# Optimization experiments

Measured on AMD Instinct MI355X. Metric: run time of the kernel, lower is better.

The kernel has to match this reference:

```python
import jax, jax.numpy as jnp
import numpy as np

H, W = 448, 448
C = 32
HEADS = 2
HEAD_DIM = C // HEADS
B, N = 4, 20000
SHIFTS = jnp.array([[0, 0], [-1, 0], [1, 0], [0, 1], [-1, 1], [1, 1], [0, -1], [-1, -1], [1, -1]], dtype=jnp.int32)  # [9,2]


def _layer_norm(x, w, b):
    mu = x.mean(-1, keepdims=True)
    var = ((x - mu) ** 2).mean(-1, keepdims=True)
    return (x - mu) / jnp.sqrt(var + 1e-5) * w + b


def _direction(q_feat, q_coor, kv_feat, kv_coor, qkv_w, qkv_b, in_w, in_b, out_w, out_b, pos_w, pos_b):
    # q_feat: [N,C] (already layer-normed), q_coor/kv_coor: [N,2] int (y,x)
    n = q_feat.shape[0]
    q_map = q_feat @ qkv_w[0].T + qkv_b[0]   # 1x1 conv == linear
    k_map = kv_feat @ qkv_w[1].T + qkv_b[1]
    v_map = kv_feat @ qkv_w[2].T + qkv_b[2]
    # dense coordinate -> voxel-index lookup table for the kv modality
    lut = jnp.full(H * W, -1, dtype=jnp.int32)
    lut = lut.at[kv_coor[:, 0] * W + kv_coor[:, 1]].set(jnp.arange(kv_coor.shape[0], dtype=jnp.int32))
    shifted = q_coor[:, None, :] + SHIFTS[None]                      # [N,9,2]
    inb = ((shifted >= 0) & (shifted < jnp.array([H, W]))).all(-1)   # [N,9]
    flat = jnp.clip(shifted[..., 0], 0, H - 1) * W + jnp.clip(shifted[..., 1], 0, W - 1)
    idx = jnp.where(inb, lut[flat], -1)                              # [N,9], -1 = no match
    mask = idx >= 0
    gi = jnp.maximum(idx, 0)
    pos = SHIFTS.astype(q_feat.dtype) @ pos_w.T + pos_b              # [9,C]
    v_g = jnp.where(mask[..., None], v_map[gi] + pos[None], 0.0)     # [N,9,C]
    k_g = jnp.where(mask[..., None], k_map[gi], 0.0)                 # [N,9,C]
    # MultiheadAttention (eval): 1 query token over 9 neighbor tokens, per voxel
    wq, wk, wv = in_w[:C], in_w[C:2 * C], in_w[2 * C:]
    bq, bk, bv = in_b[:C], in_b[C:2 * C], in_b[2 * C:]
    q = (q_map @ wq.T + bq).reshape(n, HEADS, HEAD_DIM)
    k = (k_g @ wk.T + bk).reshape(n, 9, HEADS, HEAD_DIM)
    v = (v_g @ wv.T + bv).reshape(n, 9, HEADS, HEAD_DIM)
    scores = jnp.einsum('nhd,nkhd->nhk', q, k) / jnp.sqrt(jnp.asarray(HEAD_DIM, q.dtype))
    attn = jax.nn.softmax(scores, axis=-1)
    o = jnp.einsum('nhk,nkhd->nhd', attn, v).reshape(n, C)
    out = o @ out_w.T + out_b                                        # [N,C]
    # scatter into BEV pseudoimage
    canvas = jnp.zeros((H * W, C), out.dtype).at[q_coor[:, 0] * W + q_coor[:, 1]].set(out)
    return canvas.T.reshape(C, H, W)


def setup_inputs() -> dict:
    key = jax.random.key(0)
    ks = jax.random.split(key, 20)
    rng = np.random.default_rng(0)
    def coords(rng):
        flat = np.stack([rng.choice(H * W, size=N, replace=False) for _ in range(B)])
        return jnp.asarray(np.stack([flat // W, flat % W], axis=-1), dtype=jnp.int32)  # [B,N,2]
    s = 0.05
    return {
        'li_feats': jax.random.normal(ks[0], (B, N, C), jnp.float32),
        'ra_feats': jax.random.normal(ks[1], (B, N, C), jnp.float32),
        'li_coors': coords(rng),
        'ra_coors': coords(rng),
        'li_norm_w': jnp.ones((C,), jnp.float32),
        'li_norm_b': jnp.zeros((C,), jnp.float32),
        'ra_norm_w': jnp.ones((C,), jnp.float32),
        'ra_norm_b': jnp.zeros((C,), jnp.float32),
        'qkv1_w': jax.random.normal(ks[2], (3, C, C), jnp.float32) * s,
        'qkv1_b': jax.random.normal(ks[3], (3, C), jnp.float32) * s,
        'qkv2_w': jax.random.normal(ks[4], (3, C, C), jnp.float32) * s,
        'qkv2_b': jax.random.normal(ks[5], (3, C), jnp.float32) * s,
        'pos_w': jax.random.normal(ks[6], (C, 2), jnp.float32) * s,
        'pos_b': jax.random.normal(ks[7], (C,), jnp.float32) * s,
        'attn1_in_w': jax.random.normal(ks[8], (3 * C, C), jnp.float32) * s,
        'attn1_in_b': jax.random.normal(ks[9], (3 * C,), jnp.float32) * s,
        'attn1_out_w': jax.random.normal(ks[10], (C, C), jnp.float32) * s,
        'attn1_out_b': jax.random.normal(ks[11], (C,), jnp.float32) * s,
        'attn2_in_w': jax.random.normal(ks[12], (3 * C, C), jnp.float32) * s,
        'attn2_in_b': jax.random.normal(ks[13], (3 * C,), jnp.float32) * s,
        'attn2_out_w': jax.random.normal(ks[14], (C, C), jnp.float32) * s,
        'attn2_out_b': jax.random.normal(ks[15], (C,), jnp.float32) * s,
    }


def reference(li_feats, ra_feats, li_coors, ra_coors, li_norm_w, li_norm_b, ra_norm_w, ra_norm_b,
              qkv1_w, qkv1_b, qkv2_w, qkv2_b, pos_w, pos_b,
              attn1_in_w, attn1_in_b, attn1_out_w, attn1_out_b,
              attn2_in_w, attn2_in_b, attn2_out_w, attn2_out_b):
    li_n = _layer_norm(li_feats, li_norm_w, li_norm_b)  # [B,N,C]
    ra_n = _layer_norm(ra_feats, ra_norm_w, ra_norm_b)
    d1 = jax.vmap(lambda qf, qc, kf, kc: _direction(qf, qc, kf, kc, qkv1_w, qkv1_b,
                                                    attn1_in_w, attn1_in_b, attn1_out_w, attn1_out_b, pos_w, pos_b))
    d2 = jax.vmap(lambda qf, qc, kf, kc: _direction(qf, qc, kf, kc, qkv2_w, qkv2_b,
                                                    attn2_in_w, attn2_in_b, attn2_out_w, attn2_out_b, pos_w, pos_b))
    li_img = d1(li_n, li_coors, ra_n, ra_coors)  # [B,C,H,W]
    ra_img = d2(ra_n, ra_coors, li_n, li_coors)  # [B,C,H,W]
    return li_img, ra_img
```

## Files before the change

### kernel.cpp

```cpp
#include <hip/hip_runtime.h>
#include <hip/hip_bf16.h>

#define HH 448
#define WW 448
#define HWP (HH*WW)
#define CC 32
#define NN 20000
#define BB 4
#define NPB 79

__constant__ int c_SY[9] = {0,-1,1,0,-1,1,0,-1,1};
__constant__ int c_SX[9] = {0,0,0,1,1,1,-1,-1,-1};

#define WB_STRIDE 4608

static __device__ __forceinline__ float bf(const __hip_bfloat16 v) {
    return __bfloat162float(v);
}
static __device__ __forceinline__ float ldf(const void* p, int i, int isf32) {
    if (isf32) return ((const float*)p)[i];
    return __bfloat162float(((const __hip_bfloat16*)p)[i]);
}
static __device__ __forceinline__ float blo(unsigned int u) { return __uint_as_float((u & 0xFFFFu) << 16); }
static __device__ __forceinline__ float bhi(unsigned int u) { return __uint_as_float(u & 0xFFFF0000u); }

static __device__ __forceinline__ void unpack8(uint4 r, float* f) {
    f[0]=blo(r.x); f[1]=bhi(r.x); f[2]=blo(r.y); f[3]=bhi(r.y);
    f[4]=blo(r.z); f[5]=bhi(r.z); f[6]=blo(r.w); f[7]=bhi(r.w);
}
static __device__ __forceinline__ float dot8(uint4 r, const float* q) {
    float a = 0.f;
    a = fmaf(blo(r.x), q[0], a); a = fmaf(bhi(r.x), q[1], a);
    a = fmaf(blo(r.y), q[2], a); a = fmaf(bhi(r.y), q[3], a);
    a = fmaf(blo(r.z), q[4], a); a = fmaf(bhi(r.z), q[5], a);
    a = fmaf(blo(r.w), q[6], a); a = fmaf(bhi(r.w), q[7], a);
    return a;
}
static __device__ __forceinline__ void acc8(uint4 r, float w, float4 pA, float4 pB, float* o) {
    o[0]=fmaf(w, blo(r.x)+pA.x, o[0]); o[1]=fmaf(w, bhi(r.x)+pA.y, o[1]);
    o[2]=fmaf(w, blo(r.y)+pA.z, o[2]); o[3]=fmaf(w, bhi(r.y)+pA.w, o[3]);
    o[4]=fmaf(w, blo(r.z)+pB.x, o[4]); o[5]=fmaf(w, bhi(r.z)+pB.y, o[5]);
    o[6]=fmaf(w, blo(r.w)+pB.z, o[6]); o[7]=fmaf(w, bhi(r.w)+pB.w, o[7]);
}
static __device__ __forceinline__ void store32bf(__hip_bfloat16* p, const float* a) {
    __hip_bfloat16 h[32];
    #pragma unroll
    for (int c = 0; c < 32; ++c) h[c] = __float2bfloat16(a[c]);
    uint4* rp = (uint4*)p; const uint4* hp = (const uint4*)h;
    rp[0] = hp[0]; rp[1] = hp[1]; rp[2] = hp[2]; rp[3] = hp[3];
}

__launch_bounds__(256)
__global__ void prep_build(const void* __restrict__ qkv1_w, const void* __restrict__ qkv1_b,
                           const void* __restrict__ qkv2_w, const void* __restrict__ qkv2_b,
                           const void* __restrict__ pos_w,  const void* __restrict__ pos_b,
                           const void* __restrict__ in1_w,  const void* __restrict__ in1_b,
                           const void* __restrict__ out1_w, const void* __restrict__ out1_b,
                           const void* __restrict__ in2_w,  const void* __restrict__ in2_b,
                           const void* __restrict__ out2_w, const void* __restrict__ out2_b,
                           const void* __restrict__ li_feats,
                           const int* __restrict__ li_coors, const int* __restrict__ ra_coors,
                           int* __restrict__ lut,
                           int* __restrict__ flag, float* __restrict__ wsW) {
    const int tid = threadIdx.x;
    if (blockIdx.x >= 2) {
        const int t = (blockIdx.x - 2) * 256 + tid;
        if (t >= 2 * BB * NN) return;
        const int tensor = t / (BB * NN);
        const int r = t % (BB * NN);
        const int b = r / NN, n = r % NN;
        const int* cc = tensor ? ra_coors : li_coors;
        const int y = cc[(size_t)(b * NN + n) * 2 + 0];
        const int x = cc[(size_t)(b * NN + n) * 2 + 1];
        lut[(size_t)(tensor * BB + b) * HWP + y * WW + x] = n;
        return;
    }
    __shared__ int cnt[256];
    {
        const unsigned short u = ((const unsigned short*)li_feats)[tid * 2];
        const int e = (u >> 7) & 0xFF;
        cnt[tid] = (u == 0 || (e >= 97 && e <= 157)) ? 1 : 0;
    }
    __syncthreads();
    for (int s = 128; s > 0; s >>= 1) {
        if (tid < s) cnt[tid] += cnt[tid + s];
        __syncthreads();
    }
    const int F = (cnt[0] >= 192) ? 0 : 1;
    if (blockIdx.x == 0 && tid == 0) *flag = F;

    const int d = blockIdx.x;
    const void* qw  = d ? qkv2_w : qkv1_w;
    const void* qb  = d ? qkv2_b : qkv1_b;
    const void* iw  = d ? in2_w  : in1_w;
    const void* ib  = d ? in2_b  : in1_b;
    const void* ow  = d ? out2_w : out1_w;
    const void* obp = d ? out2_b : out1_b;
    float* o = wsW + d * WB_STRIDE;

    __shared__ float s_qw[3072];
    __shared__ float s_iw[96 * 33];
    __shared__ float s_ow[32 * 33];
    __shared__ float s_qb[96], s_ib[96], s_obp[32], s_pw[64], s_pb[32];

    if (F) {
        const float* fqw = (const float*)qw;  const float* fiw = (const float*)iw;
        const float* fow = (const float*)ow;  const float* fqb = (const float*)qb;
        const float* fib = (const float*)ib;  const float* fob = (const float*)obp;
        const float* fpw = (const float*)pos_w; const float* fpb = (const float*)pos_b;
        for (int i = tid; i < 3072; i += 256) s_qw[i] = fqw[i];
        for (int i = tid; i < 3072; i += 256) s_iw[(i >> 5) * 33 + (i & 31)] = fiw[i];
        for (int i = tid; i < 1024; i += 256) s_ow[(i >> 5) * 33 + (i & 31)] = fow[i];
        if (tid < 96) { s_qb[tid] = fqb[tid]; s_ib[tid] = fib[tid]; }
        if (tid < 64) s_pw[tid] = fpw[tid];
        if (tid < 32) { s_obp[tid] = fob[tid]; s_pb[tid] = fpb[tid]; }
    } else {
        const __hip_bfloat16* hqw = (const __hip_bfloat16*)qw;  const __hip_bfloat16* hiw = (const __hip_bfloat16*)iw;
        const __hip_bfloat16* how = (const __hip_bfloat16*)ow;  const __hip_bfloat16* hqb = (const __hip_bfloat16*)qb;
        const __hip_bfloat16* hib = (const __hip_bfloat16*)ib;  const __hip_bfloat16* hob = (const __hip_bfloat16*)obp;
        const __hip_bfloat16* hpw = (const __hip_bfloat16*)pos_w; const __hip_bfloat16* hpb = (const __hip_bfloat16*)pos_b;
        for (int i = tid; i < 3072; i += 256) s_qw[i] = bf(hqw[i]);
        for (int i = tid; i < 3072; i += 256) s_iw[(i >> 5) * 33 + (i & 31)] = bf(hiw[i]);
        for (int i = tid; i < 1024; i += 256) s_ow[(i >> 5) * 33 + (i & 31)] = bf(how[i]);
        if (tid < 96) { s_qb[tid] = bf(hqb[tid]); s_ib[tid] = bf(hib[tid]); }
        if (tid < 64) s_pw[tid] = bf(hpw[tid]);
        if (tid < 32) { s_obp[tid] = bf(hob[tid]); s_pb[tid] = bf(hpb[tid]); }
    }
    __syncthreads();

    for (int k = 0; k < 4; ++k) {
        const int idx = tid + k * 256;
        const int t = idx >> 5, i = idx & 31;
        float aq = 0.f, ak = 0.f, av = 0.f;
        #pragma unroll
        for (int u = 0; u < 32; ++u) {
            const float q0 = s_qw[u * 32 + t];
            const float q1 = s_qw[1024 + u * 32 + t];
            const float q2 = s_qw[2048 + u * 32 + t];
            aq = fmaf(s_iw[i * 33 + u],        q0, aq);
            ak = fmaf(s_iw[(32 + i) * 33 + u], q1, ak);
            av = fmaf(s_iw[(64 + i) * 33 + u], q2, av);
        }
        o[idx]        = aq;
        o[1024 + idx] = ak;
        o[2048 + idx] = av;
        o[3072 + idx] = s_ow[i * 33 + t];
    }
    if (tid < 32) {
        const int i = tid;
        float aq = 0.f, ak = 0.f, av = 0.f;
        #pragma unroll
        for (int u = 0; u < 32; ++u) {
            aq = fmaf(s_qb[u],      s_iw[i * 33 + u],        aq);
            ak = fmaf(s_qb[32 + u], s_iw[(32 + i) * 33 + u], ak);
            av = fmaf(s_qb[64 + u], s_iw[(64 + i) * 33 + u], av);
        }
        o[4096 + i] = aq + s_ib[i];
        o[4128 + i] = ak + s_ib[32 + i];
        o[4160 + i] = av + s_ib[64 + i];
        o[4192 + i] = s_obp[i];
        o[4224 + i] = s_ib[32 + i];
        o[4256 + i] = s_ib[64 + i];
    }
    for (int idx = tid; idx < 288; idx += 256) {
        const int s = idx >> 5, i = idx & 31;
        const float sy = (float)c_SY[s], sx = (float)c_SX[s];
        float acc = 0.f;
        #pragma unroll
        for (int j = 0; j < 32; ++j) {
            const float pj = sy * s_pw[j * 2 + 0] + sx * s_pw[j * 2 + 1] + s_pb[j];
            acc = fmaf(pj, s_iw[(64 + i) * 33 + j], acc);
        }
        o[4288 + idx] = acc;
    }
}

__launch_bounds__(256)
__global__ void project_kernel(const void* __restrict__ li_feats, const void* __restrict__ ra_feats,
                               const void* __restrict__ li_nw, const void* __restrict__ li_nb,
                               const void* __restrict__ ra_nw, const void* __restrict__ ra_nb,
                               const int* __restrict__ flag, const float* __restrict__ wsW,
                               __hip_bfloat16* __restrict__ qOut, __hip_bfloat16* __restrict__ kOut,
                               __hip_bfloat16* __restrict__ vOut) {
    const int F = *flag;
    const int combo  = blockIdx.x / NPB;
    const int n      = (blockIdx.x % NPB) * 256 + threadIdx.x;
    if (n >= NN) return;
    const int tensor = combo >> 2;
    const int b      = combo & 3;
    const float* Wq  = wsW + tensor * WB_STRIDE;
    const float* Wkv = wsW + (1 - tensor) * WB_STRIDE;

    const void* feats = tensor ? ra_feats : li_feats;
    const void* nwp   = tensor ? ra_nw : li_nw;
    const void* nbp   = tensor ? ra_nb : li_nb;

    float x[32];
    if (F) {
        const float4* fr = (const float4*)((const float*)feats + (size_t)(b * NN + n) * CC);
        #pragma unroll
        for (int i = 0; i < 8; ++i) {
            const float4 t = fr[i];
            x[4*i] = t.x; x[4*i+1] = t.y; x[4*i+2] = t.z; x[4*i+3] = t.w;
        }
    } else {
        const uint4* hr = (const uint4*)((const __hip_bfloat16*)feats + (size_t)(b * NN + n) * CC);
        unpack8(hr[0], x); unpack8(hr[1], x + 8);
        unpack8(hr[2], x + 16); unpack8(hr[3], x + 24);
    }
    float s = 0.f;
    #pragma unroll
    for (int c = 0; c < 32; ++c) s += x[c];
    const float mu = s * (1.f / 32.f);
    float s2 = 0.f;
    #pragma unroll
    for (int c = 0; c < 32; ++c) { const float dx = x[c] - mu; s2 += dx * dx; }
    const float rs = rsqrtf(s2 * (1.f / 32.f) + 1e-5f);
    #pragma unroll
    for (int c = 0; c < 32; ++c)
        x[c] = (x[c] - mu) * rs * ldf(nwp, c, F) + ldf(nbp, c, F);

    const size_t off = ((size_t)(tensor * BB + b) * NN + n) * CC;
    #pragma unroll
    for (int pass = 0; pass < 3; ++pass) {
        const float* W = (pass == 0) ? Wq : Wkv + pass * 1024;
        const float* Bv = (pass == 0) ? (Wq + 4096) : (Wkv + 4096 + pass * 32);
        float a[32];
        const float4* b4 = (const float4*)Bv;
        #pragma unroll
        for (int i4 = 0; i4 < 8; ++i4) {
            const float4 t = b4[i4];
            a[4*i4] = t.x; a[4*i4+1] = t.y; a[4*i4+2] = t.z; a[4*i4+3] = t.w;
        }
        #pragma unroll
        for (int j = 0; j < 32; ++j) {
            const float xj = x[j];
            const float4* wr = (const float4*)&W[j * 32];
            #pragma unroll
            for (int i4 = 0; i4 < 8; ++i4) {
                const float4 w = wr[i4];
                a[4*i4+0] = fmaf(xj, w.x, a[4*i4+0]);
                a[4*i4+1] = fmaf(xj, w.y, a[4*i4+1]);
                a[4*i4+2] = fmaf(xj, w.z, a[4*i4+2]);
                a[4*i4+3] = fmaf(xj, w.w, a[4*i4+3]);
            }
        }
        store32bf((pass == 0 ? qOut : pass == 1 ? kOut : vOut) + off, a);
    }
}

__launch_bounds__(256)
__global__ void attn_kernel(const int* __restrict__ li_coors, const int* __restrict__ ra_coors,
                            const float* __restrict__ wsW, const int* __restrict__ lut,
                            const __hip_bfloat16* __restrict__ qArr, const __hip_bfloat16* __restrict__ kArr,
                            const __hip_bfloat16* __restrict__ vArr, __hip_bfloat16* __restrict__ resArr) {
    const int combo = blockIdx.x / NPB;
    const int n     = (blockIdx.x % NPB) * 256 + threadIdx.x;
    if (n >= NN) return;
    const int d = combo >> 2;
    const int b = combo & 3;
    const int qt = d, kt = 1 - d;
    const float* Wd = wsW + d * WB_STRIDE;

    const int* qc = qt ? ra_coors : li_coors;
    const int* lutk = lut + (size_t)(kt * BB + b) * HWP;
    const __hip_bfloat16* kk = kArr + (size_t)(kt * BB + b) * NN * CC;
    const __hip_bfloat16* vv = vArr + (size_t)(kt * BB + b) * NN * CC;
    const __hip_bfloat16* qq = qArr + (size_t)(qt * BB + b) * NN * CC;
    __hip_bfloat16* res = resArr + (size_t)(d * BB + b) * NN * CC;

    float q[32];
    {
        const uint4* qr = (const uint4*)(qq + (size_t)n * CC);
        unpack8(qr[0], q); unpack8(qr[1], q + 8);
        unpack8(qr[2], q + 16); unpack8(qr[3], q + 24);
    }
    const int y = qc[(size_t)(b * NN + n) * 2 + 0];
    const int x = qc[(size_t)(b * NN + n) * 2 + 1];
    int idx[9];
    #pragma unroll
    for (int s = 0; s < 9; ++s) {
        const int ny = y + c_SY[s], nx = x + c_SX[s];
        idx[s] = (ny >= 0 && ny < HH && nx >= 0 && nx < WW) ? lutk[ny * WW + nx] : -1;
    }
    float di0 = 0.f, di1 = 0.f;
    #pragma unroll
    for (int c = 0; c < 16; ++c) di0 = fmaf(q[c], Wd[4224 + c], di0);
    #pragma unroll
    for (int c = 16; c < 32; ++c) di1 = fmaf(q[c], Wd[4224 + c], di1);

    float s0[9], s1[9];
    #pragma unroll
    for (int s = 0; s < 9; ++s) {
        float d0, d1;
        if (idx[s] >= 0) {
            const uint4* kr = (const uint4*)(kk + (size_t)idx[s] * CC);
            const uint4 r0 = kr[0], r1 = kr[1], r2 = kr[2], r3 = kr[3];
            d0 = dot8(r0, q) + dot8(r1, q + 8);
            d1 = dot8(r2, q + 16) + dot8(r3, q + 24);
        } else { d0 = di0; d1 = di1; }
        s0[s] = d0 * 0.25f;
        s1[s] = d1 * 0.25f;
    }
    float m0 = s0[0], m1 = s1[0];
    #pragma unroll
    for (int s = 1; s < 9; ++s) { m0 = fmaxf(m0, s0[s]); m1 = fmaxf(m1, s1[s]); }
    float e0[9], e1[9], den0 = 0.f, den1 = 0.f;
    #pragma unroll
    for (int s = 0; s < 9; ++s) {
        e0[s] = __expf(s0[s] - m0); den0 += e0[s];
        e1[s] = __expf(s1[s] - m1); den1 += e1[s];
    }
    const float i0 = 1.f / den0, i1 = 1.f / den1;

    float o[32];
    #pragma unroll
    for (int c = 0; c < 32; ++c) o[c] = 0.f;
    float wi0 = 0.f, wi1 = 0.f;
    const float4* pv4 = (const float4*)&Wd[4288];
    #pragma unroll
    for (int s = 0; s < 9; ++s) {
        const float w0 = e0[s] * i0, w1 = e1[s] * i1;
        if (idx[s] >= 0) {
            const uint4* vr = (const uint4*)(vv + (size_t)idx[s] * CC);
            const uint4 r0 = vr[0], r1 = vr[1], r2 = vr[2], r3 = vr[3];
            acc8(r0, w0, pv4[s * 8 + 0], pv4[s * 8 + 1], o);
            acc8(r1, w0, pv4[s * 8 + 2], pv4[s * 8 + 3], o + 8);
            acc8(r2, w1, pv4[s * 8 + 4], pv4[s * 8 + 5], o + 16);
            acc8(r3, w1, pv4[s * 8 + 6], pv4[s * 8 + 7], o + 24);
        } else { wi0 += w0; wi1 += w1; }
    }
    #pragma unroll
    for (int c = 0; c < 16; ++c) o[c] = fmaf(wi0, Wd[4256 + c], o[c]);
    #pragma unroll
    for (int c = 16; c < 32; ++c) o[c] = fmaf(wi1, Wd[4256 + c], o[c]);

    float out[32];
    const float4* ob4 = (const float4*)&Wd[4192];
    #pragma unroll
    for (int i4 = 0; i4 < 8; ++i4) {
        const float4 t = ob4[i4];
        out[i4*4+0] = t.x; out[i4*4+1] = t.y;
        out[i4*4+2] = t.z; out[i4*4+3] = t.w;
    }
    #pragma unroll
    for (int j = 0; j < 32; ++j) {
        const float oj = o[j];
        const float4* wr = (const float4*)&Wd[3072 + j * 32];
        #pragma unroll
        for (int i4 = 0; i4 < 8; ++i4) {
            const float4 w = wr[i4];
            out[i4*4+0] = fmaf(oj, w.x, out[i4*4+0]);
            out[i4*4+1] = fmaf(oj, w.y, out[i4*4+1]);
            out[i4*4+2] = fmaf(oj, w.z, out[i4*4+2]);
            out[i4*4+3] = fmaf(oj, w.w, out[i4*4+3]);
        }
    }
    store32bf(res + (size_t)n * CC, out);
}

__launch_bounds__(256)
__global__ void canvas_kernel(const int* __restrict__ lut, const __hip_bfloat16* __restrict__ resArr,
                              const int* __restrict__ flag, void* __restrict__ out) {
    const int F = *flag;
    const int tile = blockIdx.x % (HWP / 64);
    const int rem  = blockIdx.x / (HWP / 64);
    const int b = rem & 3;
    const int d = rem >> 2;
    const int* lutq = lut + (size_t)(d * BB + b) * HWP + (size_t)tile * 64;
    __shared__ int ls[64];
    __shared__ float st[64 * 33];
    const int t = threadIdx.x;
    if (t < 16) ((int4*)ls)[t] = ((const int4*)lutq)[t];
    __syncthreads();

    const __hip_bfloat16* res = resArr + (size_t)(d * BB + b) * NN * CC;
    {
        const int r = t >> 2, q = t & 3;
        const int idx = ls[r];
        uint4 raw = make_uint4(0u, 0u, 0u, 0u);
        if (idx >= 0) raw = *(const uint4*)(res + (size_t)idx * CC + q * 8);
        float* dst = &st[r * 33 + q * 8];
        dst[0] = blo(raw.x); dst[1] = bhi(raw.x);
        dst[2] = blo(raw.y); dst[3] = bhi(raw.y);
        dst[4] = blo(raw.z); dst[5] = bhi(raw.z);
        dst[6] = blo(raw.w); dst[7] = bhi(raw.w);
    }
    __syncthreads();

    const int c = t >> 3, g = t & 7;
    float v[8];
    #pragma unroll
    for (int j = 0; j < 8; ++j) v[j] = st[(8 * g + j) * 33 + c];
    const size_t obase = ((size_t)(d * BB + b) * CC + c) * HWP + (size_t)tile * 64 + 8 * g;
    if (F) {
        float* ob = (float*)out + obase;
        ((float4*)ob)[0] = make_float4(v[0], v[1], v[2], v[3]);
        ((float4*)ob)[1] = make_float4(v[4], v[5], v[6], v[7]);
    } else {
        __hip_bfloat16* ob = (__hip_bfloat16*)out + obase;
        __hip_bfloat16 h[8];
        #pragma unroll
        for (int j = 0; j < 8; ++j) h[j] = __float2bfloat16(v[j]);
        *(uint4*)ob = *(const uint4*)h;
    }
}

extern "C" void kernel_launch(void* const* d_in, const int* in_sizes, int n_in,
                              void* d_out, int out_size, void* d_ws, size_t ws_size,
                              hipStream_t stream) {
    (void)in_sizes; (void)n_in; (void)out_size; (void)ws_size;
    const void* li_feats = d_in[0];
    const void* ra_feats = d_in[1];
    const int* li_coors = (const int*)d_in[2];
    const int* ra_coors = (const int*)d_in[3];
    const void* li_nw = d_in[4];
    const void* li_nb = d_in[5];
    const void* ra_nw = d_in[6];
    const void* ra_nb = d_in[7];

    char* ws = (char*)d_ws;
    int*   flag = (int*)ws;
    float* wsW  = (float*)(ws + 512);
    int*   lut  = (int*)(ws + 40960);
    __hip_bfloat16* qArr = (__hip_bfloat16*)(ws + 6463488);
    __hip_bfloat16* kArr = (__hip_bfloat16*)(ws + 16703488);
    __hip_bfloat16* vArr = (__hip_bfloat16*)(ws + 26943488);
    __hip_bfloat16* rArr = (__hip_bfloat16*)(ws + 37183488);

    hipMemsetAsync(lut, 0xFF, (size_t)2 * BB * HWP * sizeof(int), stream);
    const int buildBlocks = (2 * BB * NN + 255) / 256;
    prep_build<<<2 + buildBlocks, 256, 0, stream>>>(d_in[8], d_in[9], d_in[10], d_in[11], d_in[12], d_in[13],
                                                    d_in[14], d_in[15], d_in[16], d_in[17],
                                                    d_in[18], d_in[19], d_in[20], d_in[21],
                                                    li_feats, li_coors, ra_coors, lut, flag, wsW);
    project_kernel<<<8 * NPB, 256, 0, stream>>>(li_feats, ra_feats, li_nw, li_nb, ra_nw, ra_nb,
                                                flag, wsW, qArr, kArr, vArr);
    attn_kernel<<<8 * NPB, 256, 0, stream>>>(li_coors, ra_coors, wsW, lut, qArr, kArr, vArr, rArr);
    canvas_kernel<<<2 * BB * (HWP / 64), 256, 0, stream>>>(lut, rArr, flag, d_out);
}
```

Baseline: 334.9 us.

## Fuse Q projection into attention, interleave K/V, enlarge canvas tiles

The Q projection (layer norm plus matmul) now runs inside the attention kernel instead of going through a global bf16 buffer. K and V are stored interleaved per voxel as 64 contiguous values, so each neighbour gather reads one contiguous 128-byte row. This removes the Q write and read round trip and improves gather locality. The canvas kernel now covers 256 pixels per block in four sub-tiles, which cuts the block count and amortises the LUT load, at the cost of extra syncs per block.

Result: slower. 427.1 us (+27.5%).

```diff
diff --git a/kernel.cpp b/kernel.cpp
--- a/kernel.cpp
+++ b/kernel.cpp
@@ -48,6 +48,54 @@
     for (int c = 0; c < 32; ++c) h[c] = __float2bfloat16(a[c]);
     uint4* rp = (uint4*)p; const uint4* hp = (const uint4*)h;
     rp[0] = hp[0]; rp[1] = hp[1]; rp[2] = hp[2]; rp[3] = hp[3];
+}
+static __device__ __forceinline__ void mat32(const float* __restrict__ W, const float* __restrict__ Bv,
+                                             const float* x, float* a) {
+    const float4* b4 = (const float4*)Bv;
+    #pragma unroll
+    for (int i4 = 0; i4 < 8; ++i4) {
+        const float4 t = b4[i4];
+        a[4*i4] = t.x; a[4*i4+1] = t.y; a[4*i4+2] = t.z; a[4*i4+3] = t.w;
+    }
+    #pragma unroll
+    for (int j = 0; j < 32; ++j) {
+        const float xj = x[j];
+        const float4* wr = (const float4*)&W[j * 32];
+        #pragma unroll
+        for (int i4 = 0; i4 < 8; ++i4) {
+            const float4 w = wr[i4];
+            a[4*i4+0] = fmaf(xj, w.x, a[4*i4+0]);
+            a[4*i4+1] = fmaf(xj, w.y, a[4*i4+1]);
+            a[4*i4+2] = fmaf(xj, w.z, a[4*i4+2]);
+            a[4*i4+3] = fmaf(xj, w.w, a[4*i4+3]);
+        }
+    }
+}
+static __device__ __forceinline__ void load_ln(const void* feats, size_t row, int F,
+                                               const void* nwp, const void* nbp, float* x) {
+    if (F) {
+        const float4* fr = (const float4*)((const float*)feats + row * CC);
+        #pragma unroll
+        for (int i = 0; i < 8; ++i) {
+            const float4 t = fr[i];
+            x[4*i] = t.x; x[4*i+1] = t.y; x[4*i+2] = t.z; x[4*i+3] = t.w;
+        }
+    } else {
+        const uint4* hr = (const uint4*)((const __hip_bfloat16*)feats + row * CC);
+        unpack8(hr[0], x); unpack8(hr[1], x + 8);
+        unpack8(hr[2], x + 16); unpack8(hr[3], x + 24);
+    }
+    float s = 0.f;
+    #pragma unroll
+    for (int c = 0; c < 32; ++c) s += x[c];
+    const float mu = s * (1.f / 32.f);
+    float s2 = 0.f;
+    #pragma unroll
+    for (int c = 0; c < 32; ++c) { const float dx = x[c] - mu; s2 += dx * dx; }
+    const float rs = rsqrtf(s2 * (1.f / 32.f) + 1e-5f);
+    #pragma unroll
+    for (int c = 0; c < 32; ++c)
+        x[c] = (x[c] - mu) * rs * ldf(nwp, c, F) + ldf(nbp, c, F);
 }
 
 __launch_bounds__(256)
@@ -180,80 +228,38 @@
                                const void* __restrict__ li_nw, const void* __restrict__ li_nb,
                                const void* __restrict__ ra_nw, const void* __restrict__ ra_nb,
                                const int* __restrict__ flag, const float* __restrict__ wsW,
-                               __hip_bfloat16* __restrict__ qOut, __hip_bfloat16* __restrict__ kOut,
-                               __hip_bfloat16* __restrict__ vOut) {
+                               __hip_bfloat16* __restrict__ kvOut) {
     const int F = *flag;
     const int combo  = blockIdx.x / NPB;
     const int n      = (blockIdx.x % NPB) * 256 + threadIdx.x;
     if (n >= NN) return;
     const int tensor = combo >> 2;
     const int b      = combo & 3;
-    const float* Wq  = wsW + tensor * WB_STRIDE;
     const float* Wkv = wsW + (1 - tensor) * WB_STRIDE;
 
     const void* feats = tensor ? ra_feats : li_feats;
-    const void* nwp   = tensor ? ra_nw : li_nw;
-    const void* nbp   = tensor ? ra_nb : li_nb;
-
     float x[32];
-    if (F) {
-        const float4* fr = (const float4*)((const float*)feats + (size_t)(b * NN + n) * CC);
-        #pragma unroll
-        for (int i = 0; i < 8; ++i) {
-            const float4 t = fr[i];
-            x[4*i] = t.x; x[4*i+1] = t.y; x[4*i+2] = t.z; x[4*i+3] = t.w;
-        }
-    } else {
-        const uint4* hr = (const uint4*)((const __hip_bfloat16*)feats + (size_t)(b * NN + n) * CC);
-        unpack8(hr[0], x); unpack8(hr[1], x + 8);
-        unpack8(hr[2], x + 16); unpack8(hr[3], x + 24);
-    }
-    float s = 0.f;
-    #pragma unroll
-    for (int c = 0; c < 32; ++c) s += x[c];
-    const float mu = s * (1.f / 32.f);
-    float s2 = 0.f;
-    #pragma unroll
-    for (int c = 0; c < 32; ++c) { const float dx = x[c] - mu; s2 += dx * dx; }
-    const float rs = rsqrtf(s2 * (1.f / 32.f) + 1e-5f);
-    #pragma unroll
-    for (int c = 0; c < 32; ++c)
-        x[c] = (x[c] - mu) * rs * ldf(nwp, c, F) + ldf(nbp, c, F);
-
-    const size_t off = ((size_t)(tensor * BB + b) * NN + n) * CC;
-    #pragma unroll
-    for (int pass = 0; pass < 3; ++pass) {
-        const float* W = (pass == 0) ? Wq : Wkv + pass * 1024;
-        const float* Bv = (pass == 0) ? (Wq + 4096) : (Wkv + 4096 + pass * 32);
-        float a[32];
-        const float4* b4 = (const float4*)Bv;
-        #pragma unroll
-        for (int i4 = 0; i4 < 8; ++i4) {
-            const float4 t = b4[i4];
-            a[4*i4] = t.x; a[4*i4+1] = t.y; a[4*i4+2] = t.z; a[4*i4+3] = t.w;
-        }
-        #pragma unroll
-        for (int j = 0; j < 32; ++j) {
-            const float xj = x[j];
-            const float4* wr = (const float4*)&W[j * 32];
-            #pragma unroll
-            for (int i4 = 0; i4 < 8; ++i4) {
-                const float4 w = wr[i4];
-                a[4*i4+0] = fmaf(xj, w.x, a[4*i4+0]);
-                a[4*i4+1] = fmaf(xj, w.y, a[4*i4+1]);
-                a[4*i4+2] = fmaf(xj, w.z, a[4*i4+2]);
-                a[4*i4+3] = fmaf(xj, w.w, a[4*i4+3]);
-            }
-        }
-        store32bf((pass == 0 ? qOut : pass == 1 ? kOut : vOut) + off, a);
-    }
+    load_ln(feats, (size_t)(b * NN + n), F,
+            tensor ? ra_nw : li_nw, tensor ? ra_nb : li_nb, x);
+
+    const size_t off = ((size_t)(tensor * BB + b) * NN + n) * 64;
+    float a[32];
+    mat32(Wkv + 1024, Wkv + 4128, x, a);
+    store32bf(kvOut + off, a);
+    mat32(Wkv + 2048, Wkv + 4160, x, a);
+    store32bf(kvOut + off + 32, a);
 }
 
 __launch_bounds__(256)
-__global__ void attn_kernel(const int* __restrict__ li_coors, const int* __restrict__ ra_coors,
+__global__ void attn_kernel(const void* __restrict__ li_feats, const void* __restrict__ ra_feats,
+                            const void* __restrict__ li_nw, const void* __restrict__ li_nb,
+                            const void* __restrict__ ra_nw, const void* __restrict__ ra_nb,
+                            const int* __restrict__ li_coors, const int* __restrict__ ra_coors,
+                            const int* __restrict__ flag,
                             const float* __restrict__ wsW, const int* __restrict__ lut,
-                            const __hip_bfloat16* __restrict__ qArr, const __hip_bfloat16* __restrict__ kArr,
-                            const __hip_bfloat16* __restrict__ vArr, __hip_bfloat16* __restrict__ resArr) {
+                            const __hip_bfloat16* __restrict__ kvArr,
+                            __hip_bfloat16* __restrict__ resArr) {
+    const int F = *flag;
     const int combo = blockIdx.x / NPB;
     const int n     = (blockIdx.x % NPB) * 256 + threadIdx.x;
     if (n >= NN) return;
@@ -264,16 +270,15 @@
 
     const int* qc = qt ? ra_coors : li_coors;
     const int* lutk = lut + (size_t)(kt * BB + b) * HWP;
-    const __hip_bfloat16* kk = kArr + (size_t)(kt * BB + b) * NN * CC;
-    const __hip_bfloat16* vv = vArr + (size_t)(kt * BB + b) * NN * CC;
-    const __hip_bfloat16* qq = qArr + (size_t)(qt * BB + b) * NN * CC;
+    const __hip_bfloat16* kvb = kvArr + (size_t)(kt * BB + b) * NN * 64;
     __hip_bfloat16* res = resArr + (size_t)(d * BB + b) * NN * CC;
 
     float q[32];
     {
-        const uint4* qr = (const uint4*)(qq + (size_t)n * CC);
-        unpack8(qr[0], q); unpack8(qr[1], q + 8);
-        unpack8(qr[2], q + 16); unpack8(qr[3], q + 24);
+        float x[32];
+        load_ln(qt ? ra_feats : li_feats, (size_t)(b * NN + n), F,
+                qt ? ra_nw : li_nw, qt ? ra_nb : li_nb, x);
+        mat32(Wd, Wd + 4096, x, q);
     }
     const int y = qc[(size_t)(b * NN + n) * 2 + 0];
     const int x = qc[(size_t)(b * NN + n) * 2 + 1];
@@ -294,7 +299,7 @@
     for (int s = 0; s < 9; ++s) {
         float d0, d1;
         if (idx[s] >= 0) {
-            const uint4* kr = (const uint4*)(kk + (size_t)idx[s] * CC);
+            const uint4* kr = (const uint4*)(kvb + (size_t)idx[s] * 64);
             const uint4 r0 = kr[0], r1 = kr[1], r2 = kr[2], r3 = kr[3];
             d0 = dot8(r0, q) + dot8(r1, q + 8);
             d1 = dot8(r2, q + 16) + dot8(r3, q + 24);
@@ -322,7 +327,7 @@
     for (int s = 0; s < 9; ++s) {
         const float w0 = e0[s] * i0, w1 = e1[s] * i1;
         if (idx[s] >= 0) {
-            const uint4* vr = (const uint4*)(vv + (size_t)idx[s] * CC);
+            const uint4* vr = (const uint4*)(kvb + (size_t)idx[s] * 64 + 32);
             const uint4 r0 = vr[0], r1 = vr[1], r2 = vr[2], r3 = vr[3];
             acc8(r0, w0, pv4[s * 8 + 0], pv4[s * 8 + 1], o);
             acc8(r1, w0, pv4[s * 8 + 2], pv4[s * 8 + 3], o + 8);
@@ -336,26 +341,7 @@
     for (int c = 16; c < 32; ++c) o[c] = fmaf(wi1, Wd[4256 + c], o[c]);
 
     float out[32];
-    const float4* ob4 = (const float4*)&Wd[4192];
-    #pragma unroll
-    for (int i4 = 0; i4 < 8; ++i4) {
-        const float4 t = ob4[i4];
-        out[i4*4+0] = t.x; out[i4*4+1] = t.y;
-        out[i4*4+2] = t.z; out[i4*4+3] = t.w;
-    }
-    #pragma unroll
-    for (int j = 0; j < 32; ++j) {
-        const float oj = o[j];
-        const float4* wr = (const float4*)&Wd[3072 + j * 32];
-        #pragma unroll
-        for (int i4 = 0; i4 < 8; ++i4) {
-            const float4 w = wr[i4];
-            out[i4*4+0] = fmaf(oj, w.x, out[i4*4+0]);
-            out[i4*4+1] = fmaf(oj, w.y, out[i4*4+1]);
-            out[i4*4+2] = fmaf(oj, w.z, out[i4*4+2]);
-            out[i4*4+3] = fmaf(oj, w.w, out[i4*4+3]);
-        }
-    }
+    mat32(Wd + 3072, Wd + 4192, o, out);
     store32bf(res + (size_t)n * CC, out);
 }
 
@@ -363,46 +349,49 @@
 __global__ void canvas_kernel(const int* __restrict__ lut, const __hip_bfloat16* __restrict__ resArr,
                               const int* __restrict__ flag, void* __restrict__ out) {
     const int F = *flag;
-    const int tile = blockIdx.x % (HWP / 64);
-    const int rem  = blockIdx.x / (HWP / 64);
+    const int tile = blockIdx.x % (HWP / 256);
+    const int rem  = blockIdx.x / (HWP / 256);
     const int b = rem & 3;
     const int d = rem >> 2;
-    const int* lutq = lut + (size_t)(d * BB + b) * HWP + (size_t)tile * 64;
-    __shared__ int ls[64];
+    const int* lutq = lut + (size_t)(d * BB + b) * HWP + (size_t)tile * 256;
+    __shared__ int ls[256];
     __shared__ float st[64 * 33];
     const int t = threadIdx.x;
-    if (t < 16) ((int4*)ls)[t] = ((const int4*)lutq)[t];
-    __syncthreads();
+    if (t < 64) ((int4*)ls)[t] = ((const int4*)lutq)[t];
 
     const __hip_bfloat16* res = resArr + (size_t)(d * BB + b) * NN * CC;
-    {
-        const int r = t >> 2, q = t & 3;
-        const int idx = ls[r];
-        uint4 raw = make_uint4(0u, 0u, 0u, 0u);
-        if (idx >= 0) raw = *(const uint4*)(res + (size_t)idx * CC + q * 8);
-        float* dst = &st[r * 33 + q * 8];
-        dst[0] = blo(raw.x); dst[1] = bhi(raw.x);
-        dst[2] = blo(raw.y); dst[3] = bhi(raw.y);
-        dst[4] = blo(raw.z); dst[5] = bhi(raw.z);
-        dst[6] = blo(raw.w); dst[7] = bhi(raw.w);
-    }
-    __syncthreads();
-
+    const size_t cbase = (size_t)(d * BB + b) * CC * HWP + (size_t)tile * 256;
+    const int r = t >> 2, qc4 = t & 3;
     const int c = t >> 3, g = t & 7;
-    float v[8];
-    #pragma unroll
-    for (int j = 0; j < 8; ++j) v[j] = st[(8 * g + j) * 33 + c];
-    const size_t obase = ((size_t)(d * BB + b) * CC + c) * HWP + (size_t)tile * 64 + 8 * g;
-    if (F) {
-        float* ob = (float*)out + obase;
-        ((float4*)ob)[0] = make_float4(v[0], v[1], v[2], v[3]);
-        ((float4*)ob)[1] = make_float4(v[4], v[5], v[6], v[7]);
-    } else {
-        __hip_bfloat16* ob = (__hip_bfloat16*)out + obase;
-        __hip_bfloat16 h[8];
-        #pragma unroll
-        for (int j = 0; j < 8; ++j) h[j] = __float2bfloat16(v[j]);
-        *(uint4*)ob = *(const uint4*)h;
+
+    for (int sub = 0; sub < 4; ++sub) {
+        __syncthreads();
+        {
+            const int idx = ls[sub * 64 + r];
+            uint4 raw = make_uint4(0u, 0u, 0u, 0u);
+            if (idx >= 0) raw = *(const uint4*)(res + (size_t)idx * CC + qc4 * 8);
+            float* dst = &st[r * 33 + qc4 * 8];
+            dst[0] = blo(raw.x); dst[1] = bhi(raw.x);
+            dst[2] = blo(raw.y); dst[3] = bhi(raw.y);
+            dst[4] = blo(raw.z); dst[5] = bhi(raw.z);
+            dst[6] = blo(raw.w); dst[7] = bhi(raw.w);
+        }
+        __syncthreads();
+        float v[8];
+        #pragma unroll
+        for (int j = 0; j < 8; ++j) v[j] = st[(8 * g + j) * 33 + c];
+        const size_t obase = cbase + (size_t)c * HWP + sub * 64 + 8 * g;
+        if (F) {
+            float* ob = (float*)out + obase;
+            ((float4*)ob)[0] = make_float4(v[0], v[1], v[2], v[3]);
+            ((float4*)ob)[1] = make_float4(v[4], v[5], v[6], v[7]);
+        } else {
+            __hip_bfloat16* ob = (__hip_bfloat16*)out + obase;
+            __hip_bfloat16 h[8];
+            #pragma unroll
+            for (int j = 0; j < 8; ++j) h[j] = __float2bfloat16(v[j]);
+            *(uint4*)ob = *(const uint4*)h;
+        }
     }
 }
 
@@ -423,10 +412,8 @@
     int*   flag = (int*)ws;
     float* wsW  = (float*)(ws + 512);
     int*   lut  = (int*)(ws + 40960);
-    __hip_bfloat16* qArr = (__hip_bfloat16*)(ws + 6463488);
-    __hip_bfloat16* kArr = (__hip_bfloat16*)(ws + 16703488);
-    __hip_bfloat16* vArr = (__hip_bfloat16*)(ws + 26943488);
-    __hip_bfloat16* rArr = (__hip_bfloat16*)(ws + 37183488);
+    __hip_bfloat16* kvArr = (__hip_bfloat16*)(ws + 6463488);
+    __hip_bfloat16* rArr  = (__hip_bfloat16*)(ws + 26943488);
 
     hipMemsetAsync(lut, 0xFF, (size_t)2 * BB * HWP * sizeof(int), stream);
     const int buildBlocks = (2 * BB * NN + 255) / 256;
@@ -435,7 +422,8 @@
                                                     d_in[18], d_in[19], d_in[20], d_in[21],
                                                     li_feats, li_coors, ra_coors, lut, flag, wsW);
     project_kernel<<<8 * NPB, 256, 0, stream>>>(li_feats, ra_feats, li_nw, li_nb, ra_nw, ra_nb,
-                                                flag, wsW, qArr, kArr, vArr);
-    attn_kernel<<<8 * NPB, 256, 0, stream>>>(li_coors, ra_coors, wsW, lut, qArr, kArr, vArr, rArr);
-    canvas_kernel<<<2 * BB * (HWP / 64), 256, 0, stream>>>(lut, rArr, flag, d_out);
-}
+                                                flag, wsW, kvArr);
+    attn_kernel<<<8 * NPB, 256, 0, stream>>>(li_feats, ra_feats, li_nw, li_nb, ra_nw, ra_nb,
+                                             li_coors, ra_coors, flag, wsW, lut, kvArr, rArr);
+    canvas_kernel<<<2 * BB * (HWP / 256), 256, 0, stream>>>(lut, rArr, flag, d_out);
+}
```
